# Kernel tuning notes

Measured on AMD Instinct MI355X. Metric: run time of the kernel, lower is better.

## Reference

```python
import jax, jax.numpy as jnp
import numpy as np

B, S, E, P, H, F = 4, 4096, 256, 32, 8, 1024
DH = E // H
LN_EPS = 1e-5


def setup_inputs() -> dict:
    key = jax.random.key(0)
    ks = jax.random.split(key, 12)
    dt = jnp.float32
    return {
        "src": jax.random.normal(ks[0], (B, S, E), dt),
        "pos_embed": jax.random.normal(ks[1], (B, P, S), dt),
        # learnable positional transform (pos_linear: P -> P)
        "Wpos": jax.random.normal(ks[2], (P, P), dt) * (1.0 / np.sqrt(P)),
        "bpos": jnp.zeros((P,), dt),
        # RBF kernel hyperparameters (ScaleKernel(RBFKernel)) -- positive scalars
        "lengthscale": jnp.full((), 2.0, dt),
        "outputscale": jnp.full((), 1.0, dt),
        # value / output projections of multihead attention
        "Wv": jax.random.normal(ks[3], (E, E), dt) * (1.0 / np.sqrt(E)),
        "bv": jnp.zeros((E,), dt),
        "Wo": jax.random.normal(ks[4], (E, E), dt) * (1.0 / np.sqrt(E)),
        "bo": jnp.zeros((E,), dt),
        # feed-forward
        "W1": jax.random.normal(ks[5], (F, E), dt) * (1.0 / np.sqrt(E)),
        "b1": jnp.zeros((F,), dt),
        "W2": jax.random.normal(ks[6], (E, F), dt) * (1.0 / np.sqrt(F)),
        "b2": jnp.zeros((E,), dt),
        # layer norms
        "ln1_g": jnp.ones((E,), dt), "ln1_b": jnp.zeros((E,), dt),
        "ln2_g": jnp.ones((E,), dt), "ln2_b": jnp.zeros((E,), dt),
    }


def _layer_norm(x, g, b):
    mu = jnp.mean(x, -1, keepdims=True)
    var = jnp.mean(jnp.square(x - mu), -1, keepdims=True)
    return (x - mu) * jax.lax.rsqrt(var + LN_EPS) * g + b


def _rbf_scores(x, lengthscale, outputscale):
    # x: [B, S, P] -> scaled RBF kernel matrix [B, S, S]
    xs = x / lengthscale
    sq = jnp.sum(xs * xs, axis=-1)  # [B, S]
    d2 = sq[:, :, None] + sq[:, None, :] - 2.0 * jnp.einsum('bsp,btp->bst', xs, xs)
    d2 = jnp.maximum(d2, 0.0)
    return outputscale * jnp.exp(-0.5 * d2)


def reference(src, pos_embed, Wpos, bpos, lengthscale, outputscale,
              Wv, bv, Wo, bo, W1, b1, W2, b2, ln1_g, ln1_b, ln2_g, ln2_b):
    b, s, e = src.shape
    # learnable positional transform: [B,P,S] -> [B,S,P] -> linear -> back
    pe = jnp.einsum('bps,op->bos', pos_embed, Wpos) + bpos[None, :, None]  # [B,P,S]
    # GP-kernel attention scores over sequence positions
    scores = _rbf_scores(pe.transpose(0, 2, 1), lengthscale, outputscale)  # [B,S,S]
    attn = jax.nn.softmax(scores, axis=-1)
    # value projection, per-head weighted sum (scores shared across heads)
    v = (src @ Wv.T + bv).reshape(b, s, H, DH)
    ctx = jnp.einsum('bqk,bkhd->bqhd', attn, v).reshape(b, s, e)
    attn_out = ctx @ Wo.T + bo
    x = _layer_norm(src + attn_out, ln1_g, ln1_b)
    ff = jax.nn.relu(x @ W1.T + b1) @ W2.T + b2
    return _layer_norm(x + ff, ln2_g, ln2_b)
```

## Files before the change

kernel.cpp:

```cpp
#include <hip/hip_runtime.h>
#include <stdint.h>

#define BN 4
#define SN 4096
#define EN 256
#define PN 32
#define FN 1024
#define BS (BN*SN)
#define PAUG 64

typedef uint16_t bf16_t;
typedef short v4s  __attribute__((ext_vector_type(4)));
typedef short v8s  __attribute__((ext_vector_type(8)));
typedef __bf16 bf16x8 __attribute__((ext_vector_type(8)));
typedef float v4f   __attribute__((ext_vector_type(4)));
typedef float v16f  __attribute__((ext_vector_type(16)));

#define MFMA16(a,b,c) __builtin_amdgcn_mfma_f32_16x16x32_bf16(a,b,c,0,0,0)
#define MFMA32(a,b,c) __builtin_amdgcn_mfma_f32_32x32x16_bf16(a,b,c,0,0,0)

__device__ __forceinline__ float b2f(bf16_t x){
    uint32_t u = ((uint32_t)x) << 16; float f; __builtin_memcpy(&f, &u, 4); return f;
}
__device__ __forceinline__ bf16_t f2b(float f){
    uint32_t u; __builtin_memcpy(&u, &f, 4);
    u += 0x7FFFu + ((u >> 16) & 1u);
    return (bf16_t)(u >> 16);
}
__device__ __forceinline__ bf16x8 ldb8(const bf16_t* p){
    v8s r = *(const v8s*)p; return __builtin_bit_cast(bf16x8, r);
}
__device__ __forceinline__ bf16x8 ldb8u(const bf16_t* p){
    v4s lo = *(const v4s*)p;
    v4s hi = *(const v4s*)(p + 4);
    v8s r = __builtin_shufflevector(lo, hi, 0,1,2,3,4,5,6,7);
    return __builtin_bit_cast(bf16x8, r);
}
__device__ __forceinline__ float ldsc(const float* p){ return *p; }
__device__ __forceinline__ float ldsc(const bf16_t* p){ return b2f(*p); }
__device__ __forceinline__ void stsc(float* p, float v){ *p = v; }
__device__ __forceinline__ void stsc(bf16_t* p, float v){ *p = f2b(v); }

#if __has_builtin(__builtin_amdgcn_exp2f)
__device__ __forceinline__ float fexp2(float x){ return __builtin_amdgcn_exp2f(x); }
#else
__device__ __forceinline__ float fexp2(float x){ return exp2f(x); }
#endif

#if __has_builtin(__builtin_amdgcn_cvt_pk_bf16_f32)
typedef __bf16 bf16x2 __attribute__((ext_vector_type(2)));
__device__ __forceinline__ uint32_t pkbf16(float a, float b){
    bf16x2 r = __builtin_amdgcn_cvt_pk_bf16_f32(a, b);
    return __builtin_bit_cast(uint32_t, r);
}
#else
__device__ __forceinline__ uint32_t pkbf16(float a, float b){
    return (uint32_t)f2b(a) | ((uint32_t)f2b(b) << 16);
}
#endif

typedef const __attribute__((address_space(1))) uint32_t* glds_gp;
typedef __attribute__((address_space(3))) uint32_t* glds_lp;
__device__ __forceinline__ void glds16(const bf16_t* g, bf16_t* l){
    __builtin_amdgcn_global_load_lds((glds_gp)g, (glds_lp)l, 16, 0, 0);
}

__global__ __launch_bounds__(256) void prep_kernel(
    const float* __restrict__ src, bf16_t* __restrict__ srcb,
    const float* __restrict__ Wv, bf16_t* __restrict__ Wvb,
    const float* __restrict__ Wo, bf16_t* __restrict__ Wob,
    const float* __restrict__ W1, bf16_t* __restrict__ W1b,
    const float* __restrict__ W2, bf16_t* __restrict__ W2b,
    const float* __restrict__ pos, const float* __restrict__ Wp,
    const float* __restrict__ bp,  const float* __restrict__ lsp,
    bf16_t* __restrict__ xk, bf16_t* __restrict__ xq)
{
    __shared__ float Wsh[PN*PN];
    __shared__ float bsh[PN];
    int bid = blockIdx.x;
    int tid = threadIdx.x;

    if (bid < 4736){
        const float* sp; bf16_t* dp; int off;
        if (bid < 4096){ sp = src; dp = srcb; off = (bid*256 + tid)*4; }
        else {
            int i = ((bid - 4096)*256 + tid)*4;
            if      (i <  65536){ sp=Wv; dp=Wvb; off=i; }
            else if (i < 131072){ sp=Wo; dp=Wob; off=i- 65536; }
            else if (i < 393216){ sp=W1; dp=W1b; off=i-131072; }
            else                { sp=W2; dp=W2b; off=i-393216; }
        }
        float4 f = *(const float4*)(sp + off);
        v4s o;
        o.x = (short)f2b(f.x); o.y = (short)f2b(f.y);
        o.z = (short)f2b(f.z); o.w = (short)f2b(f.w);
        *(v4s*)(dp + off) = o;
        return;
    }

    int pb = bid - 4736;
    int b  = pb >> 4;
    int s  = (pb & 15)*256 + tid;

    for (int i = tid; i < PN*PN; i += 256) Wsh[i] = Wp[i];
    if (tid < PN) bsh[tid] = bp[tid];
    __syncthreads();

    float inv_ls = 1.0f / lsp[0];
    const float c1f = 1.4426950408889634f;

    float col[PN];
    #pragma unroll
    for (int p = 0; p < PN; p++) col[p] = pos[((size_t)b*PN + p)*SN + s];

    uint16_t xb[PN], qb[PN];
    float sq = 0.f;
    #pragma unroll 4
    for (int o = 0; o < PN; o++){
        float pe = bsh[o];
        #pragma unroll
        for (int p = 0; p < PN; p++) pe += col[p] * Wsh[o*PN + p];
        float pv = pe * inv_ls;
        uint16_t h = f2b(pv);
        xb[o] = h;
        qb[o] = f2b(c1f * pv);
        float xr = b2f(h);
        sq += xr * xr;
    }

    size_t base = ((size_t)b*SN + s) * PAUG;
    v8s pk[8];
    #pragma unroll
    for (int c = 0; c < 4; c++)
        #pragma unroll
        for (int j = 0; j < 8; j++) ((short*)&pk[c])[j] = (short)xb[c*8 + j];
    #pragma unroll
    for (int c = 4; c < 8; c++)
        #pragma unroll
        for (int j = 0; j < 8; j++) ((short*)&pk[c])[j] = 0;
    ((short*)&pk[4])[0] = (short)f2b(-0.5f * sq);
    ((short*)&pk[4])[1] = (short)0x3F80;
    #pragma unroll
    for (int c = 0; c < 8; c++) *(v8s*)(xk + base + c*8) = pk[c];

    #pragma unroll
    for (int c = 0; c < 4; c++)
        #pragma unroll
        for (int j = 0; j < 8; j++) ((short*)&pk[c])[j] = (short)qb[c*8 + j];
    ((short*)&pk[4])[0] = (short)f2b(c1f);
    ((short*)&pk[4])[1] = (short)f2b(-0.5f * sq * c1f);
    #pragma unroll
    for (int c = 0; c < 8; c++) *(v8s*)(xq + base + c*8) = pk[c];
}

template<int EPI, typename OutT>
__global__ __launch_bounds__(256) void gemm_t(
    const bf16_t* __restrict__ A, const bf16_t* __restrict__ W,
    const float* __restrict__ bias, OutT* __restrict__ out,
    bf16_t* __restrict__ vt, int N, int K)
{
    __shared__ __align__(16) bf16_t At[2][4096];
    __shared__ __align__(16) bf16_t Wt[2][4096];
    int tid = threadIdx.x;
    int lane = tid & 63, wv = tid >> 6, col = lane & 15, quad = lane >> 4;
    int m0 = blockIdx.x * 64, n0 = blockIdx.y * 64;
    int nck = K >> 6;

    int srow = tid >> 3;
    int spc  = (tid & 7) ^ (srow & 7);
    const bf16_t* asrc = A + (size_t)(m0 + srow)*K + spc*8;
    const bf16_t* wsrc = W + (size_t)(n0 + srow)*K + spc*8;

    v4f acc[4];
    #pragma unroll
    for (int t = 0; t < 4; t++) acc[t] = (v4f){0.f,0.f,0.f,0.f};

    glds16(asrc, &At[0][tid*8]);
    glds16(asrc + (size_t)32*K, &At[0][2048 + tid*8]);
    glds16(wsrc, &Wt[0][tid*8]);
    glds16(wsrc + (size_t)32*K, &Wt[0][2048 + tid*8]);
    __syncthreads();

    for (int c = 0; c < nck; c++){
        int cb = c & 1;
        if (c + 1 < nck){
            glds16(asrc + (c+1)*64, &At[cb^1][tid*8]);
            glds16(asrc + (size_t)32*K + (c+1)*64, &At[cb^1][2048 + tid*8]);
            glds16(wsrc + (c+1)*64, &Wt[cb^1][tid*8]);
            glds16(wsrc + (size_t)32*K + (c+1)*64, &Wt[cb^1][2048 + tid*8]);
        }
        #pragma unroll
        for (int kc = 0; kc < 2; kc++){
            int pc = ((kc*4 + quad) ^ (col & 7)) * 8;
            bf16x8 a = ldb8(&At[cb][(wv*16 + col)*64 + pc]);
            #pragma unroll
            for (int t = 0; t < 4; t++){
                bf16x8 b = ldb8(&Wt[cb][(t*16 + col)*64 + pc]);
                acc[t] = MFMA16(a, b, acc[t]);
            }
        }
        __syncthreads();
    }

    float bfv[4];
    #pragma unroll
    for (int t = 0; t < 4; t++) bfv[t] = bias[n0 + t*16 + col];

    if constexpr (EPI == 3){
        __shared__ uint16_t Tsh[64*74];
        #pragma unroll
        for (int r = 0; r < 4; r++)
            #pragma unroll
            for (int t = 0; t < 4; t++)
                Tsh[(wv*16 + quad*4 + r)*74 + t*16 + col] = f2b(acc[t][r] + bfv[t]);
        __syncthreads();
        int e = tid >> 2, sc = tid & 3;
        int b = m0 >> 12;
        int sbat = m0 & (SN-1);
        int eb   = (n0 + e) >> 5;
        int l31e = (n0 + e) & 31;
        int k16  = (sbat >> 4) + sc;
        v8s p0, p1;
        #pragma unroll
        for (int i = 0; i < 8; i++) ((short*)&p0)[i] = (short)Tsh[(sc*16 + i)*74 + e];
        #pragma unroll
        for (int i = 0; i < 8; i++) ((short*)&p1)[i] = (short)Tsh[(sc*16 + 8 + i)*74 + e];
        bf16_t* dst = vt + ((((size_t)b*8 + eb)*256 + k16)*64 + l31e)*8;
        *(v8s*)dst = p0;
        *(v8s*)(dst + 256) = p1;
    } else {
        #pragma unroll
        for (int r = 0; r < 4; r++){
            int row = m0 + wv*16 + quad*4 + r;
            #pragma unroll
            for (int t = 0; t < 4; t++){
                float y = acc[t][r] + bfv[t];
                if constexpr (EPI == 1) y = fmaxf(y, 0.f);
                stsc(out + (size_t)row*N + n0 + t*16 + col, y);
            }
        }
    }
}

template<typename OutT, typename ResT>
__global__ __launch_bounds__(256) void ln_kernel(
    const bf16_t* __restrict__ y, const ResT* __restrict__ res,
    const float* __restrict__ gamma, const float* __restrict__ beta,
    OutT* __restrict__ out)
{
    int tid = threadIdx.x;
    int row = blockIdx.x * 32 + (tid >> 3);
    int l8  = tid & 7;
    size_t base = (size_t)row * EN;
    float v[32];
    float s1 = 0.f, s2 = 0.f;
    #pragma unroll
    for (int i = 0; i < 4; i++){
        int off = l8*8 + i*64;
        v8s a = *(const v8s*)(y + base + off);
        #pragma unroll
        for (int j = 0; j < 8; j++){
            float t = b2f((bf16_t)(uint16_t)a[j]) + ldsc(res + base + off + j);
            v[i*8 + j] = t; s1 += t; s2 += t*t;
        }
    }
    #pragma unroll
    for (int m = 1; m <= 4; m <<= 1){
        s1 += __shfl_xor(s1, m);
        s2 += __shfl_xor(s2, m);
    }
    float mu = s1 * (1.f/256.f);
    float rs = rsqrtf(s2 * (1.f/256.f) - mu*mu + 1e-5f);
    #pragma unroll
    for (int i = 0; i < 4; i++){
        int off = l8*8 + i*64;
        #pragma unroll
        for (int j = 0; j < 8; j++)
            stsc(out + base + off + j, (v[i*8+j]-mu)*rs*gamma[off+j] + beta[off+j]);
    }
}

__global__ __launch_bounds__(512, 4) void attn_kernel(
    const bf16_t* __restrict__ xk, const bf16_t* __restrict__ xq,
    const bf16_t* __restrict__ vf, const float* __restrict__ osp,
    bf16_t* __restrict__ ctx)
{
    __shared__ __align__(16) bf16_t Wtb[2][64*132];
    __shared__ __align__(16) bf16_t Qs[64*64];
    __shared__ float densh[8][64];
    __shared__ float dent[64];

    int tid  = threadIdx.x;
    int lane = tid & 63;
    int wv   = tid >> 6;
    int col  = lane & 15;
    int quad = lane >> 4;
    int l31  = lane & 31;
    int half = lane >> 5;

    int bid = blockIdx.x;
    int b   = (bid & 7) >> 1;
    int qi  = ((bid >> 3) << 1) | (bid & 1);
    int q0  = qi * 64;

    float k2 = 1.4426950408889634f * osp[0];

    const bf16_t* xkb = xk + (size_t)b * SN * PAUG;
    const bf16_t* xqb = xq + (size_t)b * SN * PAUG;
    const bf16_t* vfb = vf + (((size_t)b*8 + wv)*256)*512 + lane*8;

    {
        int qrow = tid >> 3;
        int qpc  = (tid & 7) ^ (qrow & 7);
        glds16(xqb + (size_t)(q0 + qrow)*PAUG + qpc*8, &Qs[tid*8]);
    }

    v16f acc[2];
    #pragma unroll
    for (int qg = 0; qg < 2; qg++)
        #pragma unroll
        for (int i = 0; i < 16; i++) acc[qg][i] = 0.f;
    float den[4] = {0.f, 0.f, 0.f, 0.f};
    const v4f zero = (v4f){0.f,0.f,0.f,0.f};

    bf16x8 kf0, kf1;
    {
        const bf16_t* kr = xkb + (size_t)(wv*16 + col)*PAUG + quad*8;
        kf0 = ldb8(kr); kf1 = ldb8(kr + 32);
    }

    __syncthreads();

    for (int c = 0; c < 32; c++){
        int cb = c & 1;
        bf16x8 vr[8];
        #pragma unroll
        for (int sk = 0; sk < 8; sk++)
            vr[sk] = ldb8(vfb + (size_t)(c*8 + sk)*512);

        #pragma unroll
        for (int qg = 0; qg < 2; qg++){
            #pragma unroll
            for (int g2 = 0; g2 < 2; g2++){
                int qr = qg*32 + g2*16 + col;
                bf16x8 qa = ldb8(&Qs[qr*64 + ((quad    ) ^ (col & 7))*8]);
                bf16x8 qb = ldb8(&Qs[qr*64 + ((4 + quad) ^ (col & 7))*8]);
                v4f st = MFMA16(kf0, qa, zero);
                st = MFMA16(kf1, qb, st);
                #pragma unroll
                for (int rp = 0; rp < 2; rp++){
                    float w0 = fexp2(fmaf(k2, fexp2(st[rp*2+0]), -k2));
                    float w1 = fexp2(fmaf(k2, fexp2(st[rp*2+1]), -k2));
                    den[qg*2+g2] += w0 + w1;
                    *(uint32_t*)&Wtb[cb][qr*132 + wv*16 + quad*4 + rp*2]
                        = pkbf16(w0, w1);
                }
            }
        }

        if (c + 1 < 32){
            const bf16_t* kr = xkb + (size_t)((c+1)*128 + wv*16 + col)*PAUG + quad*8;
            kf0 = ldb8(kr); kf1 = ldb8(kr + 32);
        }

        asm volatile("s_waitcnt lgkmcnt(0)" ::: "memory");
        __builtin_amdgcn_s_barrier();
        __builtin_amdgcn_sched_barrier(0);

        #pragma unroll
        for (int qg = 0; qg < 2; qg++){
            #pragma unroll
            for (int sk4 = 0; sk4 < 2; sk4++){
                bf16x8 af[4];
                #pragma unroll
                for (int j = 0; j < 4; j++)
                    af[j] = ldb8u(&Wtb[cb][(qg*32 + l31)*132 + (sk4*4 + j)*16 + half*8]);
                #pragma unroll
                for (int j = 0; j < 4; j++)
                    acc[qg] = MFMA32(af[j], vr[sk4*4 + j], acc[qg]);
            }
        }
    }

    #pragma unroll
    for (int d = 0; d < 4; d++){
        den[d] += __shfl_xor(den[d], 16);
        den[d] += __shfl_xor(den[d], 32);
    }
    if (lane < 16){
        #pragma unroll
        for (int qg = 0; qg < 2; qg++)
            #pragma unroll
            for (int g2 = 0; g2 < 2; g2++)
                densh[wv][qg*32 + g2*16 + lane] = den[qg*2+g2];
    }
    __syncthreads();
    if (tid < 64){
        float s = 0.f;
        #pragma unroll
        for (int w = 0; w < 8; w++) s += densh[w][tid];
        dent[tid] = 1.f / s;
    }
    __syncthreads();

    size_t obase = ((size_t)b*SN + q0) * EN + wv*32;
    #pragma unroll
    for (int qg = 0; qg < 2; qg++){
        #pragma unroll
        for (int rg = 0; rg < 16; rg++){
            int row = (rg & 3) + 8*(rg >> 2) + 4*half;
            float inv = dent[qg*32 + row];
            ctx[obase + (size_t)(qg*32 + row)*EN + l31] = f2b(acc[qg][rg] * inv);
        }
    }
}

extern "C" void kernel_launch(void* const* d_in, const int* in_sizes, int n_in,
                              void* d_out, int out_size, void* d_ws, size_t ws_size,
                              hipStream_t stream)
{
    (void)in_sizes; (void)n_in; (void)out_size; (void)ws_size;
    const float* src  = (const float*)d_in[0];
    const float* pos  = (const float*)d_in[1];
    const float* Wpos = (const float*)d_in[2];
    const float* bpos = (const float*)d_in[3];
    const float* ls   = (const float*)d_in[4];
    const float* os   = (const float*)d_in[5];
    const float* Wv   = (const float*)d_in[6];
    const float* bv   = (const float*)d_in[7];
    const float* Wo   = (const float*)d_in[8];
    const float* bo   = (const float*)d_in[9];
    const float* W1   = (const float*)d_in[10];
    const float* b1   = (const float*)d_in[11];
    const float* W2   = (const float*)d_in[12];
    const float* b2   = (const float*)d_in[13];
    const float* g1   = (const float*)d_in[14];
    const float* be1  = (const float*)d_in[15];
    const float* g2   = (const float*)d_in[16];
    const float* be2  = (const float*)d_in[17];

    char* w = (char*)d_ws;
    bf16_t* xkb  = (bf16_t*)(w);
    bf16_t* xqb  = (bf16_t*)(w + ( 2u<<20));
    bf16_t* Wvb  = (bf16_t*)(w + ( 4u<<20));
    bf16_t* Wob  = (bf16_t*)(w + ( 4u<<20) + (1u<<18));
    bf16_t* W1b  = (bf16_t*)(w + ( 5u<<20));
    bf16_t* W2b  = (bf16_t*)(w + ( 6u<<20));
    bf16_t* srcb = (bf16_t*)(w + ( 8u<<20));
    bf16_t* y2   = (bf16_t*)(w + ( 8u<<20));
    bf16_t* vtg  = (bf16_t*)(w + (16u<<20));
    bf16_t* y1   = (bf16_t*)(w + (16u<<20));
    bf16_t* ctx  = (bf16_t*)(w + (24u<<20));
    bf16_t* xws  = (bf16_t*)(w + (24u<<20));
    bf16_t* hws  = (bf16_t*)(w + (32u<<20));

    prep_kernel<<<dim3(4800), 256, 0, stream>>>(
        src, srcb, Wv, Wvb, Wo, Wob, W1, W1b, W2, W2b,
        pos, Wpos, bpos, ls, xkb, xqb);

    gemm_t<3, bf16_t><<<dim3(BS/64, EN/64), 256, 0, stream>>>(
        srcb, Wvb, bv, (bf16_t*)nullptr, vtg, EN, EN);
    attn_kernel<<<dim3(256), 512, 0, stream>>>(xkb, xqb, vtg, os, ctx);
    gemm_t<0, bf16_t><<<dim3(BS/64, EN/64), 256, 0, stream>>>(
        ctx, Wob, bo, y1, (bf16_t*)nullptr, EN, EN);
    ln_kernel<bf16_t, bf16_t><<<dim3(BS/32), 256, 0, stream>>>(y1, srcb, g1, be1, xws);
    gemm_t<1, bf16_t><<<dim3(BS/64, FN/64), 256, 0, stream>>>(
        xws, W1b, b1, hws, (bf16_t*)nullptr, FN, EN);
    gemm_t<0, bf16_t><<<dim3(BS/64, EN/64), 256, 0, stream>>>(
        hws, W2b, b2, y2, (bf16_t*)nullptr, EN, FN);
    ln_kernel<float, bf16_t><<<dim3(BS/32), 256, 0, stream>>>(y2, xws, g2, be2, (float*)d_out);
}
```

Measured before the change: 246.1 us.

## Use 128x128 double-buffered GEMM tiles for output and FFN projections

```diff
diff --git a/kernel.cpp b/kernel.cpp
--- a/kernel.cpp
+++ b/kernel.cpp
@@ -237,6 +237,83 @@
                 float y = acc[t][r] + bfv[t];
                 if constexpr (EPI == 1) y = fmaxf(y, 0.f);
                 stsc(out + (size_t)row*N + n0 + t*16 + col, y);
+            }
+        }
+    }
+}
+
+template<int EPI>
+__global__ __launch_bounds__(256, 2) void gemm128(
+    const bf16_t* __restrict__ A, const bf16_t* __restrict__ W,
+    const float* __restrict__ bias, bf16_t* __restrict__ out,
+    int N, int K)
+{
+    __shared__ __align__(16) bf16_t At[2][8192];
+    __shared__ __align__(16) bf16_t Wt[2][8192];
+    int tid = threadIdx.x;
+    int lane = tid & 63, wv = tid >> 6, col = lane & 15, quad = lane >> 4;
+    int m0 = blockIdx.x * 128, n0 = blockIdx.y * 128;
+    int nck = K >> 6;
+
+    int srow = tid >> 3;
+    int spc  = (tid & 7) ^ (srow & 7);
+    const bf16_t* asrc = A + (size_t)(m0 + srow)*K + spc*8;
+    const bf16_t* wsrc = W + (size_t)(n0 + srow)*K + spc*8;
+
+    v4f acc[2][8];
+    #pragma unroll
+    for (int mi = 0; mi < 2; mi++)
+        #pragma unroll
+        for (int t = 0; t < 8; t++) acc[mi][t] = (v4f){0.f,0.f,0.f,0.f};
+
+    #pragma unroll
+    for (int s = 0; s < 4; s++){
+        glds16(asrc + (size_t)(s*32)*K, &At[0][s*2048 + tid*8]);
+        glds16(wsrc + (size_t)(s*32)*K, &Wt[0][s*2048 + tid*8]);
+    }
+    __syncthreads();
+
+    for (int c = 0; c < nck; c++){
+        int cb = c & 1;
+        if (c + 1 < nck){
+            #pragma unroll
+            for (int s = 0; s < 4; s++){
+                glds16(asrc + (size_t)(s*32)*K + (c+1)*64, &At[cb^1][s*2048 + tid*8]);
+                glds16(wsrc + (size_t)(s*32)*K + (c+1)*64, &Wt[cb^1][s*2048 + tid*8]);
+            }
+        }
+        #pragma unroll
+        for (int kc = 0; kc < 2; kc++){
+            int pc = ((kc*4 + quad) ^ (col & 7)) * 8;
+            bf16x8 a[2];
+            #pragma unroll
+            for (int mi = 0; mi < 2; mi++)
+                a[mi] = ldb8(&At[cb][(wv*32 + mi*16 + col)*64 + pc]);
+            #pragma unroll
+            for (int t = 0; t < 8; t++){
+                bf16x8 b = ldb8(&Wt[cb][(t*16 + col)*64 + pc]);
+                #pragma unroll
+                for (int mi = 0; mi < 2; mi++)
+                    acc[mi][t] = MFMA16(a[mi], b, acc[mi][t]);
+            }
+        }
+        __syncthreads();
+    }
+
+    float bfv[8];
+    #pragma unroll
+    for (int t = 0; t < 8; t++) bfv[t] = bias[n0 + t*16 + col];
+
+    #pragma unroll
+    for (int mi = 0; mi < 2; mi++){
+        #pragma unroll
+        for (int r = 0; r < 4; r++){
+            int row = m0 + wv*32 + mi*16 + quad*4 + r;
+            #pragma unroll
+            for (int t = 0; t < 8; t++){
+                float y = acc[mi][t][r] + bfv[t];
+                if constexpr (EPI == 1) y = fmaxf(y, 0.f);
+                out[(size_t)row*N + n0 + t*16 + col] = f2b(y);
             }
         }
     }
@@ -461,12 +538,12 @@
     gemm_t<3, bf16_t><<<dim3(BS/64, EN/64), 256, 0, stream>>>(
         srcb, Wvb, bv, (bf16_t*)nullptr, vtg, EN, EN);
     attn_kernel<<<dim3(256), 512, 0, stream>>>(xkb, xqb, vtg, os, ctx);
-    gemm_t<0, bf16_t><<<dim3(BS/64, EN/64), 256, 0, stream>>>(
-        ctx, Wob, bo, y1, (bf16_t*)nullptr, EN, EN);
+    gemm128<0><<<dim3(BS/128, EN/128), 256, 0, stream>>>(
+        ctx, Wob, bo, y1, EN, EN);
     ln_kernel<bf16_t, bf16_t><<<dim3(BS/32), 256, 0, stream>>>(y1, srcb, g1, be1, xws);
-    gemm_t<1, bf16_t><<<dim3(BS/64, FN/64), 256, 0, stream>>>(
-        xws, W1b, b1, hws, (bf16_t*)nullptr, FN, EN);
-    gemm_t<0, bf16_t><<<dim3(BS/64, EN/64), 256, 0, stream>>>(
-        hws, W2b, b2, y2, (bf16_t*)nullptr, EN, FN);
+    gemm128<1><<<dim3(BS/128, FN/128), 256, 0, stream>>>(
+        xws, W1b, b1, hws, FN, EN);
+    gemm128<0><<<dim3(BS/128, EN/128), 256, 0, stream>>>(
+        hws, W2b, b2, y2, EN, FN);
     ln_kernel<float, bf16_t><<<dim3(BS/32), 256, 0, stream>>>(y2, xws, g2, be2, (float*)d_out);
 }
```

New measurement: 248.9 us. No clear change (+1.1%).
